# Kernel tuning notes

Hardware: AMD Instinct MI355X
Metric: run time of the kernel (lower is better)

## Reference

```python
import jax, jax.numpy as jnp
import numpy as np

B, T, D = 2, 2048, 2048
H, HD = 16, 128          # n_heads, head_dim = d_out // n_heads
DC, DR = 512, 64         # latent dim d_c, rope dim d_R


def _rope(x):
    """RoPE over last dim (even), positions along axis -2. x: [..., T, Dr]."""
    half = x.shape[-1] // 2
    t = x.shape[-2]
    inv_freq = 1.0 / (10000.0 ** (jnp.arange(half, dtype=jnp.float32) / half))
    freqs = jnp.arange(t, dtype=jnp.float32)[:, None] * inv_freq[None, :]  # [T, half]
    sin, cos = jnp.sin(freqs), jnp.cos(freqs)
    x1, x2 = x[..., :half], x[..., half:]
    # stack pairs on a new last axis then flatten -> interleaved layout,
    # matching torch.stack((...), dim=-1) followed by implicit flatten
    rot = jnp.stack([x1 * cos - x2 * sin, x1 * sin + x2 * cos], axis=-1)
    return rot.reshape(x.shape[:-1] + (2 * half,))


def setup_inputs() -> dict:
    key = jax.random.key(0)
    ks = jax.random.split(key, 10)
    s = 0.02  # init scale
    return {
        "x":     jax.random.normal(ks[0], (B, T, D), dtype=jnp.float32),
        "W_DKV": jax.random.normal(ks[1], (D, DC), dtype=jnp.float32) * s,
        "W_DQ":  jax.random.normal(ks[2], (D, DC), dtype=jnp.float32) * s,
        "W_UK":  jax.random.normal(ks[3], (DC, D), dtype=jnp.float32) * s,
        "W_UV":  jax.random.normal(ks[4], (DC, D), dtype=jnp.float32) * s,
        "W_UQ":  jax.random.normal(ks[5], (DC, D), dtype=jnp.float32) * s,
        "W_KR":  jax.random.normal(ks[6], (D, DR), dtype=jnp.float32) * s,
        "W_QR":  jax.random.normal(ks[7], (DC, H * DR), dtype=jnp.float32) * s,
        "W_O":   jax.random.normal(ks[8], (D, D), dtype=jnp.float32) * s,
        "b_O":   jax.random.normal(ks[9], (D,), dtype=jnp.float32) * s,
    }


def reference(x, W_DKV, W_DQ, W_UK, W_UV, W_UQ, W_KR, W_QR, W_O, b_O):
    b, t, d = x.shape
    # latent KV compression and up-projection
    c_kv = x @ W_DKV                                        # [B,T,d_c]
    K = (c_kv @ W_UK).reshape(b, t, H, HD).transpose(0, 2, 1, 3)  # [B,H,T,hd]
    V = (c_kv @ W_UV).reshape(b, t, H, HD).transpose(0, 2, 1, 3)
    # latent Q compression and up-projection
    c_q = x @ W_DQ                                          # [B,T,d_c]
    Q = (c_q @ W_UQ).reshape(b, t, H, HD).transpose(0, 2, 1, 3)
    # decoupled RoPE channels: shared rotary key per token, per-head rotary query
    k_R = _rope(x @ W_KR)[:, None, :, :]                    # [B,1,T,d_R]
    k_R = jnp.broadcast_to(k_R, (b, H, t, DR))
    q_R = (c_q @ W_QR).reshape(b, t, H, DR).transpose(0, 2, 1, 3)  # [B,H,T,d_R]
    q_R = _rope(q_R)
    # concat content + rotary channels
    Kf = jnp.concatenate([K, k_R], axis=-1)                 # [B,H,T,hd+d_R]
    Qf = jnp.concatenate([Q, q_R], axis=-1)
    scale = 1.0 / jnp.sqrt(jnp.float32(HD + DR))
    scores = jnp.einsum('bhqd,bhkd->bhqk', Qf, Kf) * scale  # [B,H,T,T]
    attn = jax.nn.softmax(scores, axis=-1)                  # dropout is identity (p=0 / eval)
    ctx = jnp.einsum('bhqk,bhkd->bhqd', attn, V)            # [B,H,T,hd]
    ctx = ctx.transpose(0, 2, 1, 3).reshape(b, t, d)
    return ctx @ W_O + b_O
```

## Files before the change

kernel.cpp:

```cpp
#include <hip/hip_runtime.h>
#include <hip/hip_bf16.h>

typedef __attribute__((ext_vector_type(8))) short short8;
typedef __attribute__((ext_vector_type(4))) short s4_t;
typedef __attribute__((ext_vector_type(4))) float f32x4;
typedef __attribute__((ext_vector_type(16))) float f32x16;
typedef __attribute__((ext_vector_type(2))) unsigned uint2v;
typedef __hip_bfloat16 bf16;

#define NB 2
#define NT 2048
#define NDIM 2048
#define NH 16
#define NHD 128
#define NDC 512
#define NDR 64

__device__ __forceinline__ void gl_lds16(const bf16* g, bf16* l){
  __builtin_amdgcn_global_load_lds(
      (const __attribute__((address_space(1))) void*)(const void*)g,
      (__attribute__((address_space(3))) void*)(void*)l, 16, 0, 0);
}

__global__ __launch_bounds__(256) void cvt_kernel(const float* __restrict__ src, bf16* __restrict__ dst){
  int i = (blockIdx.x*256 + threadIdx.x)*4;
  float4 v = *(const float4*)(src + i);
  dst[i+0] = __float2bfloat16(v.x);
  dst[i+1] = __float2bfloat16(v.y);
  dst[i+2] = __float2bfloat16(v.z);
  dst[i+3] = __float2bfloat16(v.w);
}

__global__ __launch_bounds__(256) void tconv_kernel(const float* __restrict__ W, bf16* __restrict__ Wt, int K, int N){
  __shared__ float tile[32][33];
  int n0 = blockIdx.x*32, k0 = blockIdx.y*32;
  int tx = threadIdx.x & 31, ty = threadIdx.x >> 5;
  #pragma unroll
  for (int j=0;j<32;j+=8) tile[ty+j][tx] = W[(size_t)(k0+ty+j)*N + n0 + tx];
  __syncthreads();
  #pragma unroll
  for (int j=0;j<32;j+=8) Wt[(size_t)(n0+ty+j)*K + k0 + tx] = __float2bfloat16(tile[tx][ty+j]);
}

template<int MODE>
__global__ __launch_bounds__(256,3) void gemm_bt(const bf16* __restrict__ A,
    const bf16* __restrict__ Bt, bf16* __restrict__ C, float* __restrict__ Cf,
    const float* __restrict__ bias, int M, int N, int K, int lda, int Tq, int Dpad, float mult)
{
  __shared__ bf16 As[128*64];
  __shared__ bf16 Bs[128*64];
  const int m0 = blockIdx.x*128, n0 = blockIdx.y*128;
  const int t = threadIdx.x, lane = t&63, w = t>>6;
  const int wr = w>>1, wc = w&1;
  const int l15 = lane&15, lg = lane>>4;
  const int wbase = t & 192;

  f32x4 acc[4][4];
  #pragma unroll
  for (int mi=0;mi<4;mi++)
    #pragma unroll
    for (int nj=0;nj<4;nj++) acc[mi][nj] = (f32x4){0.f,0.f,0.f,0.f};

  for (int k0=0;k0<K;k0+=64){
    __syncthreads();
    #pragma unroll
    for (int j=0;j<4;j++){
      int c = j*256 + t;
      int r = c>>3, cc = (c&7)*8;
      gl_lds16(A + (size_t)(m0+r)*lda + k0 + cc, As + (size_t)(j*256 + wbase)*8);
      int bn = n0 + r; if (bn > N-1) bn = N-1;
      gl_lds16(Bt + (size_t)bn*K + k0 + cc, Bs + (size_t)(j*256 + wbase)*8);
    }
    __syncthreads();
    #pragma unroll
    for (int kk=0;kk<2;kk++){
      short8 af[4], bfv[4];
      #pragma unroll
      for (int mi=0;mi<4;mi++) af[mi] = *(const short8*)&As[(wr*64+mi*16+l15)*64 + kk*32+lg*8];
      #pragma unroll
      for (int nj=0;nj<4;nj++) bfv[nj] = *(const short8*)&Bs[(wc*64+nj*16+l15)*64 + kk*32+lg*8];
      #pragma unroll
      for (int mi=0;mi<4;mi++)
        #pragma unroll
        for (int nj=0;nj<4;nj++)
          acc[mi][nj] = __builtin_amdgcn_mfma_f32_16x16x32_bf16(af[mi], bfv[nj], acc[mi][nj], 0,0,0);
    }
  }

  #pragma unroll
  for (int mi=0;mi<4;mi++){
    #pragma unroll
    for (int nj=0;nj<4;nj++){
      f32x4 v = acc[mi][nj];
      int gr0 = m0 + wr*64 + mi*16 + lg*4;
      int gc  = n0 + wc*64 + nj*16 + l15;
      if constexpr (MODE==0){
        if (gc < N){
          #pragma unroll
          for (int r2=0;r2<4;r2++) C[(size_t)(gr0+r2)*N + gc] = __float2bfloat16(v[r2]*mult);
        }
      } else if constexpr (MODE==1){
        int bidx = m0 / Tq;
        int hq = gc >> 7, dl = gc & 127;
        int Hn = N >> 7;
        size_t base = ((size_t)bidx*Hn + hq)*(size_t)Tq;
        int tl0 = (m0 % Tq) + wr*64 + mi*16 + lg*4;
        #pragma unroll
        for (int r2=0;r2<4;r2++) C[(base + tl0 + r2)*Dpad + dl] = __float2bfloat16(v[r2]*mult);
      } else if constexpr (MODE==3){
        int bidx = gr0 >> 11;
        int tl0 = gr0 & 2047;
        int hq = gc >> 7, dl = gc & 127;
        s4_t pk;
        #pragma unroll
        for (int r2=0;r2<4;r2++){
          union { bf16 b; unsigned short u; } cvu;
          cvu.b = __float2bfloat16(v[r2]*mult);
          pk[r2] = (short)cvu.u;
        }
        *(s4_t*)&C[(((size_t)bidx*NH + hq)*NHD + dl)*NT + tl0] = pk;
      } else {
        float bb = bias[gc];
        #pragma unroll
        for (int r2=0;r2<4;r2++) Cf[(size_t)(gr0+r2)*N + gc] = v[r2]*mult + bb;
      }
    }
  }
}

__global__ __launch_bounds__(128) void rope_kernel(const bf16* __restrict__ krp,
    const bf16* __restrict__ qrp, bf16* __restrict__ Kf, bf16* __restrict__ Qf)
{
  int bt = blockIdx.x*2 + (threadIdx.x>>6);
  int d = threadIdx.x & 63;
  int b = bt >> 11, tpos = bt & 2047;
  int i = d >> 1;
  const float scale = 0.07216878364870323f;
  float inv = __expf(-(float)i * 0.2878231366242557f);
  float fr = (float)tpos * inv;
  float sn, cs;
  sincosf(fr, &sn, &cs);

  float x1 = __bfloat162float(krp[(size_t)bt*1088 + i]);
  float x2 = __bfloat162float(krp[(size_t)bt*1088 + 32 + i]);
  float kv = (d&1) ? (x1*sn + x2*cs) : (x1*cs - x2*sn);
  bf16 kvb = __float2bfloat16(kv);
  size_t base = ((size_t)b*NH*NT + tpos)*192;
  #pragma unroll
  for (int h=0;h<NH;h++) Kf[base + (size_t)h*NT*192 + 128 + d] = kvb;

  #pragma unroll
  for (int h=0;h<NH;h++){
    float y1 = __bfloat162float(qrp[bt*1024 + h*64 + i]);
    float y2 = __bfloat162float(qrp[bt*1024 + h*64 + 32 + i]);
    float qv = (d&1) ? (y1*sn + y2*cs) : (y1*cs - y2*sn);
    Qf[base + (size_t)h*NT*192 + 128 + d] = __float2bfloat16(qv*scale);
  }
}

static __device__ inline void plswap(unsigned &a, unsigned &b){
  uint2v r = __builtin_amdgcn_permlane32_swap(a, b, false, false);
  a = r[0]; b = r[1];
}
static __device__ inline unsigned cvtpk(float lo, float hi){
  unsigned u;
  asm("v_cvt_pk_bf16_f32 %0, %1, %2" : "=v"(u) : "v"(lo), "v"(hi));
  return u;
}

__global__ __launch_bounds__(256,2) void attn_kernel(const bf16* __restrict__ Qf,
    const bf16* __restrict__ Kf, const bf16* __restrict__ Vt, bf16* __restrict__ ctx)
{
  __shared__ __align__(16) char smem[40960];
  char* KsB  = smem;
  char* VTsB = smem + 24576;

  const int lin = blockIdx.x;
  const int swz = (lin & 7)*64 + (lin >> 3);
  const int qt = swz & 15, bh = swz >> 4;
  const int b = bh >> 4, h = bh & 15;
  const int q0 = qt * 128;
  const int t = threadIdx.x, lane = t&63, w = t>>6;
  const int l31 = lane&31, hi = lane>>5;
  const int rsw = (l31&7)<<4;
  const int hib = hi*16;

  const bf16* Qp  = Qf + ((size_t)bh*NT + q0)*192;
  const bf16* Kp  = Kf + (size_t)bh*NT*192;
  const bf16* Vtp = Vt + (size_t)bh*NHD*NT;

  short8 qf[12];
  #pragma unroll
  for (int kk=0;kk<12;kk++)
    qf[kk] = *(const short8*)(Qp + (size_t)(w*32 + l31)*192 + kk*16 + hi*8);

  f32x16 o[4];
  #pragma unroll
  for (int Dt=0;Dt<4;Dt++)
    #pragma unroll
    for (int r=0;r<16;r++) o[Dt][r] = 0.f;
  float mrun = -1e30f, lrun = 0.f;

  short8 kst[6], vst[4];
  auto load_tile = [&](int kt){
    const bf16* Ksrc = Kp + (size_t)kt*64*192;
    #pragma unroll
    for (int j=0;j<6;j++) kst[j] = *(const short8*)(Ksrc + (j*256+t)*8);
    #pragma unroll
    for (int j=0;j<4;j++){
      int c = j*256 + t;
      vst[j] = *(const short8*)(Vtp + (size_t)(c>>3)*NT + kt*64 + (c&7)*8);
    }
  };
  load_tile(0);

  for (int kt=0; kt<NT/64; kt++){
    __syncthreads();
    #pragma unroll
    for (int j=0;j<6;j++){
      int c = j*256 + t;
      int r = c/24, cb = (c%24)*16;
      *(short8*)(KsB + r*384 + (cb ^ ((r&7)<<4))) = kst[j];
    }
    #pragma unroll
    for (int j=0;j<4;j++){
      int c = j*256 + t;
      int r = c>>3, cb = (c&7)*16;
      *(short8*)(VTsB + r*128 + (cb ^ ((r&7)<<4))) = vst[j];
    }
    __syncthreads();
    if (kt+1 < NT/64) load_tile(kt+1);

    f32x16 sa[2];
    #pragma unroll
    for (int Mt=0;Mt<2;Mt++)
      #pragma unroll
      for (int r=0;r<16;r++) sa[Mt][r] = 0.f;
    #pragma unroll
    for (int kk=0;kk<12;kk++){
      int cb = kk*32 + hib;
      short8 kf0 = *(const short8*)(KsB + (size_t)l31*384        + ((cb) ^ rsw));
      short8 kf1 = *(const short8*)(KsB + (size_t)(l31+32)*384   + ((cb) ^ rsw));
      sa[0] = __builtin_amdgcn_mfma_f32_32x32x16_bf16(kf0, qf[kk], sa[0], 0,0,0);
      sa[1] = __builtin_amdgcn_mfma_f32_32x32x16_bf16(kf1, qf[kk], sa[1], 0,0,0);
    }

    float mx[8];
    #pragma unroll
    for (int i2=0;i2<8;i2++)
      mx[i2] = fmaxf(fmaxf(sa[0][2*i2], sa[0][2*i2+1]), fmaxf(sa[1][2*i2], sa[1][2*i2+1]));
    float tm = fmaxf(fmaxf(fmaxf(mx[0],mx[1]),fmaxf(mx[2],mx[3])),
                     fmaxf(fmaxf(mx[4],mx[5]),fmaxf(mx[6],mx[7])));
    tm = fmaxf(tm, __shfl_xor(tm, 32));

    if (__any(tm > mrun + 8.f)){
      float mn = fmaxf(mrun, tm);
      float alpha = __expf(mrun - mn);
      mrun = mn;
      lrun *= alpha;
      #pragma unroll
      for (int Dt=0;Dt<4;Dt++)
        #pragma unroll
        for (int r=0;r<16;r++) o[Dt][r] *= alpha;
    }

    #pragma unroll
    for (int Mt=0;Mt<2;Mt++)
      #pragma unroll
      for (int r=0;r<16;r++) sa[Mt][r] = __expf(sa[Mt][r] - mrun);
    float sm[8];
    #pragma unroll
    for (int i2=0;i2<8;i2++)
      sm[i2] = (sa[0][2*i2] + sa[0][2*i2+1]) + (sa[1][2*i2] + sa[1][2*i2+1]);
    float rs = ((sm[0]+sm[1])+(sm[2]+sm[3])) + ((sm[4]+sm[5])+(sm[6]+sm[7]));
    rs += __shfl_xor(rs, 32);
    lrun += rs;

    short8 pf[4];
    #pragma unroll
    for (int Mt=0;Mt<2;Mt++){
      unsigned u[8];
      #pragma unroll
      for (int p8=0;p8<8;p8++) u[p8] = cvtpk(sa[Mt][2*p8], sa[Mt][2*p8+1]);
      plswap(u[0], u[2]); plswap(u[1], u[3]);
      plswap(u[4], u[6]); plswap(u[5], u[7]);
      union { unsigned du[4]; short8 s8; } f0, f1;
      f0.du[0]=u[0]; f0.du[1]=u[1]; f0.du[2]=u[2]; f0.du[3]=u[3];
      f1.du[0]=u[4]; f1.du[1]=u[5]; f1.du[2]=u[6]; f1.du[3]=u[7];
      pf[2*Mt+0] = f0.s8;
      pf[2*Mt+1] = f1.s8;
    }

    #pragma unroll
    for (int kw=0;kw<4;kw++){
      int cb = kw*32 + hib;
      #pragma unroll
      for (int Dt=0;Dt<4;Dt++){
        short8 vf = *(const short8*)(VTsB + (size_t)(Dt*32 + l31)*128 + ((cb) ^ rsw));
        o[Dt] = __builtin_amdgcn_mfma_f32_32x32x16_bf16(vf, pf[kw], o[Dt], 0,0,0);
      }
    }
  }

  __syncthreads();
  float il = 1.0f / lrun;
  bf16* Es = (bf16*)smem;
  const int EROW = 136;
  const int ebase = w*32*EROW;
  #pragma unroll
  for (int Dt=0;Dt<4;Dt++)
    #pragma unroll
    for (int r=0;r<16;r++){
      int d = Dt*32 + (r&3) + 8*(r>>2) + 4*hi;
      Es[ebase + l31*EROW + d] = __float2bfloat16(o[Dt][r]*il);
    }
  __syncthreads();
  int q = lane>>1, halfd = lane&1;
  size_t gq = q0 + w*32 + q;
  size_t obase = (((size_t)b*NT + gq)*NH + h)*NHD + halfd*64;
  #pragma unroll
  for (int pp=0;pp<8;pp++)
    *(short8*)&ctx[obase + pp*8] = *(short8*)&Es[ebase + q*EROW + halfd*64 + pp*8];
}

extern "C" void kernel_launch(void* const* d_in, const int* in_sizes, int n_in,
                              void* d_out, int out_size, void* d_ws, size_t ws_size,
                              hipStream_t stream)
{
  const float* x     = (const float*)d_in[0];
  const float* W_DKV = (const float*)d_in[1];
  const float* W_DQ  = (const float*)d_in[2];
  const float* W_UK  = (const float*)d_in[3];
  const float* W_UV  = (const float*)d_in[4];
  const float* W_UQ  = (const float*)d_in[5];
  const float* W_KR  = (const float*)d_in[6];
  const float* W_QR  = (const float*)d_in[7];
  const float* W_O   = (const float*)d_in[8];
  const float* b_O   = (const float*)d_in[9];

  const float scale = 0.07216878364870323f;

  char* ws = (char*)d_ws;
  bf16* xb    = (bf16*)(ws + 0);
  bf16* wcomb = (bf16*)(ws + 16777216);
  bf16* wuk   = (bf16*)(ws + 21233664);
  bf16* wuv   = (bf16*)(ws + 23330816);
  bf16* wuq   = (bf16*)(ws + 25427968);
  bf16* wqr   = (bf16*)(ws + 27525120);
  bf16* wo    = (bf16*)(ws + 28573696);
  bf16* comb  = (bf16*)(ws + 36962304);
  bf16* qrp   = (bf16*)(ws + 45875200);
  bf16* Qf    = (bf16*)(ws + 54263808);
  bf16* Kf    = (bf16*)(ws + 79429632);
  bf16* vt    = (bf16*)(ws + 104595456);
  bf16* ctxb  = (bf16*)(ws + 121372672);

  bf16* ckv = comb;
  bf16* cq  = comb + 512;
  bf16* krp = comb + 1024;

  cvt_kernel<<<8192,256,0,stream>>>(x, xb);
  tconv_kernel<<<dim3(16,64),256,0,stream>>>(W_DKV, wcomb,              2048, 512);
  tconv_kernel<<<dim3(16,64),256,0,stream>>>(W_DQ,  wcomb + 512*2048,   2048, 512);
  tconv_kernel<<<dim3(2,64), 256,0,stream>>>(W_KR,  wcomb + 1024*2048,  2048, 64);
  tconv_kernel<<<dim3(64,16),256,0,stream>>>(W_UK,  wuk,  512, 2048);
  tconv_kernel<<<dim3(64,16),256,0,stream>>>(W_UV,  wuv,  512, 2048);
  tconv_kernel<<<dim3(64,16),256,0,stream>>>(W_UQ,  wuq,  512, 2048);
  tconv_kernel<<<dim3(32,16),256,0,stream>>>(W_QR,  wqr,  512, 1024);
  tconv_kernel<<<dim3(64,64),256,0,stream>>>(W_O,   wo,   2048, 2048);

  gemm_bt<0><<<dim3(32,9), 256,0,stream>>>(xb, wcomb, comb, nullptr, nullptr, 4096, 1088, 2048, 2048, 1, 0, 1.0f);

  gemm_bt<1><<<dim3(32,16),256,0,stream>>>(ckv, wuk, Kf, nullptr, nullptr, 4096, 2048, 512, 1088, 2048, 192, 1.0f);
  gemm_bt<3><<<dim3(32,16),256,0,stream>>>(ckv, wuv, vt, nullptr, nullptr, 4096, 2048, 512, 1088, 2048, 128, 1.0f);
  gemm_bt<1><<<dim3(32,16),256,0,stream>>>(cq,  wuq, Qf, nullptr, nullptr, 4096, 2048, 512, 1088, 2048, 192, scale);
  gemm_bt<0><<<dim3(32,8), 256,0,stream>>>(cq,  wqr, qrp, nullptr, nullptr, 4096, 1024, 512, 1088, 1, 0, 1.0f);

  rope_kernel<<<2048,128,0,stream>>>(krp, qrp, Kf, Qf);
  attn_kernel<<<512,256,0,stream>>>(Qf, Kf, vt, ctxb);
  gemm_bt<2><<<dim3(32,16),256,0,stream>>>(ctxb, wo, nullptr, (float*)d_out, b_O, 4096, 2048, 2048, 2048, 1, 0, 1.0f);
}
```

Measured before the change: 296.0 us.

## Merge weight transposes into one launch and load V fragments directly from global

The eight per-weight transpose-convert launches become a single batched launch that uses a cumulative block table to pick each block's matrix. In the attention kernel, V is no longer staged through LDS: each wave loads its V MFMA fragments straight from global memory in two halves, one issued before the QK MFMAs and one after. This cuts LDS footprint and LDS write traffic and removes seven launches. In exchange, every wave re-reads the same V data from global or cache, and the 16 extra short8 registers may raise register pressure.

```diff
diff --git a/kernel.cpp b/kernel.cpp
--- a/kernel.cpp
+++ b/kernel.cpp
@@ -31,9 +31,25 @@
   dst[i+3] = __float2bfloat16(v.w);
 }
 
-__global__ __launch_bounds__(256) void tconv_kernel(const float* __restrict__ W, bf16* __restrict__ Wt, int K, int N){
+struct TAll {
+  const float* src[8];
+  bf16* dst[8];
+  int K[8];
+  int N[8];
+  int cum[9];
+};
+__global__ __launch_bounds__(256) void tconv_all(TAll a){
   __shared__ float tile[32][33];
-  int n0 = blockIdx.x*32, k0 = blockIdx.y*32;
+  int bid = blockIdx.x;
+  int i = 0;
+  #pragma unroll
+  for (int j=0;j<8;j++) if (bid >= a.cum[j+1]) i = j+1;
+  const float* W = a.src[i];
+  bf16* Wt = a.dst[i];
+  int K = a.K[i], N = a.N[i];
+  int tl = bid - a.cum[i];
+  int ntx = N >> 5;
+  int n0 = (tl % ntx)*32, k0 = (tl / ntx)*32;
   int tx = threadIdx.x & 31, ty = threadIdx.x >> 5;
   #pragma unroll
   for (int j=0;j<32;j+=8) tile[ty+j][tx] = W[(size_t)(k0+ty+j)*N + n0 + tx];
@@ -171,9 +187,8 @@
 __global__ __launch_bounds__(256,2) void attn_kernel(const bf16* __restrict__ Qf,
     const bf16* __restrict__ Kf, const bf16* __restrict__ Vt, bf16* __restrict__ ctx)
 {
-  __shared__ __align__(16) char smem[40960];
+  __shared__ __align__(16) char smem[34816];
   char* KsB  = smem;
-  char* VTsB = smem + 24576;
 
   const int lin = blockIdx.x;
   const int swz = (lin & 7)*64 + (lin >> 3);
@@ -201,18 +216,13 @@
     for (int r=0;r<16;r++) o[Dt][r] = 0.f;
   float mrun = -1e30f, lrun = 0.f;
 
-  short8 kst[6], vst[4];
-  auto load_tile = [&](int kt){
+  short8 kst[6];
+  auto load_k = [&](int kt){
     const bf16* Ksrc = Kp + (size_t)kt*64*192;
     #pragma unroll
     for (int j=0;j<6;j++) kst[j] = *(const short8*)(Ksrc + (j*256+t)*8);
-    #pragma unroll
-    for (int j=0;j<4;j++){
-      int c = j*256 + t;
-      vst[j] = *(const short8*)(Vtp + (size_t)(c>>3)*NT + kt*64 + (c&7)*8);
-    }
   };
-  load_tile(0);
+  load_k(0);
 
   for (int kt=0; kt<NT/64; kt++){
     __syncthreads();
@@ -222,14 +232,16 @@
       int r = c/24, cb = (c%24)*16;
       *(short8*)(KsB + r*384 + (cb ^ ((r&7)<<4))) = kst[j];
     }
-    #pragma unroll
-    for (int j=0;j<4;j++){
-      int c = j*256 + t;
-      int r = c>>3, cb = (c&7)*16;
-      *(short8*)(VTsB + r*128 + (cb ^ ((r&7)<<4))) = vst[j];
-    }
     __syncthreads();
-    if (kt+1 < NT/64) load_tile(kt+1);
+    if (kt+1 < NT/64) load_k(kt+1);
+
+    const bf16* Vsrc = Vtp + kt*64 + hi*8;
+    short8 vA[8], vB[8];
+    #pragma unroll
+    for (int kw=0;kw<2;kw++)
+      #pragma unroll
+      for (int Dt=0;Dt<4;Dt++)
+        vA[kw*4+Dt] = *(const short8*)(Vsrc + (size_t)(Dt*32+l31)*NT + kw*16);
 
     f32x16 sa[2];
     #pragma unroll
@@ -244,6 +256,12 @@
       sa[0] = __builtin_amdgcn_mfma_f32_32x32x16_bf16(kf0, qf[kk], sa[0], 0,0,0);
       sa[1] = __builtin_amdgcn_mfma_f32_32x32x16_bf16(kf1, qf[kk], sa[1], 0,0,0);
     }
+
+    #pragma unroll
+    for (int kw=0;kw<2;kw++)
+      #pragma unroll
+      for (int Dt=0;Dt<4;Dt++)
+        vB[kw*4+Dt] = *(const short8*)(Vsrc + (size_t)(Dt*32+l31)*NT + (kw+2)*16);
 
     float mx[8];
     #pragma unroll
@@ -293,10 +311,9 @@
 
     #pragma unroll
     for (int kw=0;kw<4;kw++){
-      int cb = kw*32 + hib;
       #pragma unroll
       for (int Dt=0;Dt<4;Dt++){
-        short8 vf = *(const short8*)(VTsB + (size_t)(Dt*32 + l31)*128 + ((cb) ^ rsw));
+        short8 vf = (kw<2) ? vA[kw*4+Dt] : vB[(kw-2)*4+Dt];
         o[Dt] = __builtin_amdgcn_mfma_f32_32x32x16_bf16(vf, pf[kw], o[Dt], 0,0,0);
       }
     }
@@ -360,14 +377,19 @@
   bf16* krp = comb + 1024;
 
   cvt_kernel<<<8192,256,0,stream>>>(x, xb);
-  tconv_kernel<<<dim3(16,64),256,0,stream>>>(W_DKV, wcomb,              2048, 512);
-  tconv_kernel<<<dim3(16,64),256,0,stream>>>(W_DQ,  wcomb + 512*2048,   2048, 512);
-  tconv_kernel<<<dim3(2,64), 256,0,stream>>>(W_KR,  wcomb + 1024*2048,  2048, 64);
-  tconv_kernel<<<dim3(64,16),256,0,stream>>>(W_UK,  wuk,  512, 2048);
-  tconv_kernel<<<dim3(64,16),256,0,stream>>>(W_UV,  wuv,  512, 2048);
-  tconv_kernel<<<dim3(64,16),256,0,stream>>>(W_UQ,  wuq,  512, 2048);
-  tconv_kernel<<<dim3(32,16),256,0,stream>>>(W_QR,  wqr,  512, 1024);
-  tconv_kernel<<<dim3(64,64),256,0,stream>>>(W_O,   wo,   2048, 2048);
+
+  TAll ta;
+  ta.src[0]=W_DKV; ta.dst[0]=wcomb;             ta.K[0]=2048; ta.N[0]=512;
+  ta.src[1]=W_DQ;  ta.dst[1]=wcomb + 512*2048;  ta.K[1]=2048; ta.N[1]=512;
+  ta.src[2]=W_KR;  ta.dst[2]=wcomb + 1024*2048; ta.K[2]=2048; ta.N[2]=64;
+  ta.src[3]=W_UK;  ta.dst[3]=wuk;               ta.K[3]=512;  ta.N[3]=2048;
+  ta.src[4]=W_UV;  ta.dst[4]=wuv;               ta.K[4]=512;  ta.N[4]=2048;
+  ta.src[5]=W_UQ;  ta.dst[5]=wuq;               ta.K[5]=512;  ta.N[5]=2048;
+  ta.src[6]=W_QR;  ta.dst[6]=wqr;               ta.K[6]=512;  ta.N[6]=1024;
+  ta.src[7]=W_O;   ta.dst[7]=wo;                ta.K[7]=2048; ta.N[7]=2048;
+  ta.cum[0]=0;
+  for (int i=0;i<8;i++) ta.cum[i+1] = ta.cum[i] + (ta.N[i]/32)*(ta.K[i]/32);
+  tconv_all<<<ta.cum[8],256,0,stream>>>(ta);
 
   gemm_bt<0><<<dim3(32,9), 256,0,stream>>>(xb, wcomb, comb, nullptr, nullptr, 4096, 1088, 2048, 2048, 1, 0, 1.0f);
 
```

Result: slower. 370.2 us (+25.1%).
